# Kernel tuning notes

Measured on AMD Instinct MI355X. Metric: run time of the kernel, lower is better.

Reference implementation:

```python
import jax, jax.numpy as jnp
import numpy as np

N = 20000; E = 160000; C = 64; SH = 9; NB = 8
S_DIM = 16; MS_HID = 64; FC_HID = 64
RATE = 0.1; LAMBDA = 0.5; R_MAX = 5.0; EV_PER = 16
K = int(RATE * N)          # static master-node count (top-k selection)
E_V = EV_PER * K           # static virtual-edge budget


def _safe_len(vec):
    # smooth norm, safe under autodiff at zero-length edges (self loops)
    return jnp.sqrt(jnp.sum(vec * vec, axis=-1, keepdims=True) + 1e-12)


def _sh(vec):
    # real spherical harmonics lmax=2, 'component' normalization, on unit vectors
    n = vec / _safe_len(vec)
    x, y, z = n[:, 0], n[:, 1], n[:, 2]
    s3 = jnp.sqrt(3.0); s15 = jnp.sqrt(15.0); s5 = jnp.sqrt(5.0)
    return jnp.stack([
        jnp.ones_like(x),
        s3 * x, s3 * y, s3 * z,
        s15 * x * y, s15 * y * z, 0.5 * s5 * (3 * z * z - 1.0),
        s15 * x * z, 0.5 * s15 * (x * x - y * y),
    ], axis=-1)  # [E, 9]


def _bessel(r):
    # Bessel radial basis with p=6 polynomial cutoff envelope; r: [E,1]
    n = jnp.arange(1, NB + 1, dtype=r.dtype)
    b = jnp.sqrt(2.0 / R_MAX) * jnp.sin(n * jnp.pi * r / R_MAX) / jnp.clip(r, 1e-9)
    u = jnp.clip(r / R_MAX, 0.0, 1.0); p = 6.0
    env = 1.0 - (p + 1) * (p + 2) / 2 * u ** p + p * (p + 2) * u ** (p + 1) - p * (p + 1) / 2 * u ** (p + 2)
    return b * env  # [E, NB]


def _conv(h, src, dst, sh, ef, emask, n_nodes, fc_w1, fc_b1, fc_w2, fc_b2, lin_w):
    # TFN-style tensor-product conv: per-edge weights from radial MLP,
    # message = flatten(h[dst] outer sh) * w -> linear -> scatter-mean to src
    w = jax.nn.relu(ef @ fc_w1 + fc_b1) @ fc_w2 + fc_b2            # [E, C*SH]
    tp = (h[dst][:, :, None] * sh[:, None, :]).reshape(sh.shape[0], -1) * w
    msg = (tp @ lin_w) * emask[:, None]                            # [E, C]
    agg = jax.ops.segment_sum(msg, src, num_segments=n_nodes)
    deg = jax.ops.segment_sum(emask, src, num_segments=n_nodes)
    return agg / jnp.clip(deg, 1.0)[:, None]


def setup_inputs() -> dict:
    key = jax.random.key(0)
    ks = jax.random.split(key, 12)
    def lin(k, i, o):
        return (jax.random.normal(k, (i, o), jnp.float32) / np.sqrt(i)).astype(jnp.float32)
    return {
        "h": jax.random.normal(ks[0], (N, C), jnp.float32),
        "pos": jax.random.uniform(ks[1], (N, 3), jnp.float32) * 10.0,
        "edge_index": jax.random.randint(ks[2], (2, E), 0, N, dtype=jnp.int32),
        "fc_w1": lin(ks[3], NB, FC_HID), "fc_b1": jnp.zeros((FC_HID,), jnp.float32),
        "fc_w2": lin(ks[4], FC_HID, C * SH), "fc_b2": jnp.zeros((C * SH,), jnp.float32),
        "lin_w": lin(ks[5], C * SH, C),
        "ms_w1": lin(ks[6], S_DIM, MS_HID), "ms_b1": jnp.zeros((MS_HID,), jnp.float32),
        "ms_w2": lin(ks[7], MS_HID, 1), "ms_b2": jnp.zeros((1,), jnp.float32),
        "vg_wq": lin(ks[8], S_DIM, S_DIM), "vg_wk": lin(ks[9], S_DIM, S_DIM),
    }


def reference(h, pos, fc_w1, fc_b1, fc_w2, fc_b2, lin_w,
              ms_w1, ms_b1, ms_w2, ms_b2, vg_wq, vg_wk, edge_index):
    src, dst = edge_index[0], edge_index[1]
    vec = pos[src] - pos[dst]
    sh = _sh(vec)
    ef = _bessel(_safe_len(vec))
    ones_e = jnp.ones((E,), h.dtype)
    h_update = _conv(h, src, dst, sh, ef, ones_e, N, fc_w1, fc_b1, fc_w2, fc_b2, lin_w)
    h_local = h_update + h  # in_dim == out_dim -> pad is a no-op

    # --- master selection (top-k by learned score; static K) ---
    h_sc = h_local[:, :S_DIM]
    score = jax.nn.sigmoid(
        (jax.nn.relu(h_sc @ ms_w1 + ms_b1) @ ms_w2 + ms_b2).squeeze(-1))  # [N]
    _, top_idx = jax.lax.top_k(score, K)
    node_mask = jnp.zeros((N,), h.dtype).at[top_idx].set(1.0)
    m = score * node_mask
    master_idx = jnp.sort(top_idx)

    # relabel full-graph ids -> master-subgraph ids (masked subgraph extraction)
    node2m = jnp.full((N,), -1, jnp.int32).at[master_idx].set(jnp.arange(K, dtype=jnp.int32))
    src_m, dst_m = node2m[src], node2m[dst]
    e_mask = ((src_m >= 0) & (dst_m >= 0)).astype(h.dtype)
    src_mc = jnp.where(src_m >= 0, src_m, 0)
    dst_mc = jnp.where(dst_m >= 0, dst_m, 0)
    adj = jnp.zeros((K, K), h.dtype).at[src_mc, dst_mc].add(e_mask)

    h_master = h_local[master_idx]
    pos_master = pos[master_idx]
    h_ms = h_master[:, :S_DIM]

    # --- virtual edge generation (attention, thresholded by lambda) ---
    q = h_ms @ vg_wq; kk = h_ms @ vg_wk
    attn = jax.nn.sigmoid(q @ kk.T / np.sqrt(S_DIM))  # [K, K]
    exist = (adj > 0) | jnp.eye(K, dtype=bool)
    A_virtual = jnp.where((~exist) & (attn > LAMBDA), 1.0, 0.0).astype(h.dtype)
    vvals, vidx = jax.lax.top_k((attn * A_virtual).reshape(-1), E_V)
    v_src = (vidx // K).astype(jnp.int32); v_dst = (vidx % K).astype(jnp.int32)
    v_mask = (vvals > 0).astype(h.dtype)

    src_all = jnp.concatenate([src_mc, v_src])
    dst_all = jnp.concatenate([dst_mc, v_dst])
    mask_all = jnp.concatenate([e_mask, v_mask])
    vec_m = pos_master[src_all] - pos_master[dst_all]
    sh_m = _sh(vec_m)
    ef_m = _bessel(_safe_len(vec_m))
    h_m_update = _conv(h_master, src_all, dst_all, sh_m, ef_m, mask_all, K,
                       fc_w1, fc_b1, fc_w2, fc_b2, lin_w)
    h_hier = h_m_update + h_master

    h_hier_exp = jnp.zeros_like(h_local).at[master_idx].set(h_hier)
    m_e = m[:, None]
    h_final = (1.0 - m_e) * h_local + m_e * h_hier_exp
    return (h_final, pos, A_virtual, m)
```

## Files before the change

### kernel.cpp

```cpp
#include <hip/hip_runtime.h>
#include <stdint.h>

constexpr int N_   = 20000;
constexpr int E_   = 160000;
constexpr int C_   = 64;
constexpr int K_   = 2000;
constexpr int EV_  = 32000;
constexpr int EALL_ = E_ + EV_;
constexpr int CSH_ = 576;
constexpr int TB_  = 48;

constexpr size_t OFF_AGG    = 0;
constexpr size_t OFF_DEG    = 5120000;
constexpr size_t OFF_AGGM   = 5200000;
constexpr size_t OFF_DEGM   = 5712000;
constexpr size_t OFF_RANK   = 5720000;
constexpr size_t OFF_MASKA  = 5800000;
constexpr size_t OFF_EXIST  = 6568000;
constexpr size_t OFF_HIST   = 10568000;
constexpr size_t OFF_STATE  = 10572096;
constexpr size_t ZERO_BYTES = 10572352;
constexpr size_t OFF_HLOCAL = 10572352;
constexpr size_t OFF_KEY    = 15692352;
constexpr size_t OFF_SCORE  = 15852352;
constexpr size_t OFF_N2M    = 15932352;
constexpr size_t OFF_MIDX   = 16012352;
constexpr size_t OFF_HM     = 16020352;
constexpr size_t OFF_POSM   = 16532352;
constexpr size_t OFF_Q      = 16556352;
constexpr size_t OFF_KBUF   = 16684352;
constexpr size_t OFF_SRCA   = 16812352;
constexpr size_t OFF_DSTA   = 17580352;
constexpr size_t OFF_TMAX   = 18348352;
constexpr size_t OFF_CAND   = 18410880;

struct RState {
    unsigned long long prefix;
    int R;
    unsigned int cand_count;
    unsigned int sel_count;
    int bin_thresh;
    unsigned int total;
    unsigned int pad;
};

__global__ void k_w0(const float* __restrict__ fc_b1, const float* __restrict__ fc_w2,
                     const float* __restrict__ fc_b2, int* __restrict__ w0nz)
{
    __shared__ float hid0[64];
    __shared__ int nz;
    int tid = threadIdx.x;
    if (tid == 0) nz = 0;
    if (tid < 64) hid0[tid] = fmaxf(fc_b1[tid], 0.0f);
    __syncthreads();
    if (tid < CSH_) {
        float acc = fc_b2[tid];
        for (int k = 0; k < 64; k++) acc += hid0[k] * fc_w2[k * CSH_ + tid];
        if (acc != 0.0f) atomicOr(&nz, 1);
    }
    __syncthreads();
    if (tid == 0) *w0nz = nz;
}

__global__ __launch_bounds__(256) void k_prep(
    int n_edges, const int* __restrict__ src, const int* __restrict__ dst,
    const float* __restrict__ mask, const float* __restrict__ posn,
    const int* __restrict__ w0nz, float* __restrict__ deg,
    float* __restrict__ edata, unsigned int* __restrict__ cnt)
{
    int e = blockIdx.x * 256 + threadIdx.x;
    bool valid = e < n_edges;
    int s_i = 0, d_i = 0; float msk = 0.0f;
    if (valid) {
        msk = mask ? mask[e] : 1.0f;
        if (msk != 0.0f) { s_i = src[e]; d_i = dst[e]; }
    }
    bool active = valid && (msk != 0.0f);

    float vx = 0.f, vy = 0.f, vz = 0.f;
    if (active) {
        vx = posn[s_i*3+0] - posn[d_i*3+0];
        vy = posn[s_i*3+1] - posn[d_i*3+1];
        vz = posn[s_i*3+2] - posn[d_i*3+2];
    }
    float r = sqrtf(vx*vx + vy*vy + vz*vz + 1e-12f);
    float invr = 1.0f / r;
    float x = vx*invr, y = vy*invr, z = vz*invr;
    const float s3 = 1.7320508075688772f, s15 = 3.872983346207417f, s5 = 2.23606797749979f;
    float sh[9];
    sh[0] = 1.0f; sh[1] = s3*x; sh[2] = s3*y; sh[3] = s3*z;
    sh[4] = s15*x*y; sh[5] = s15*y*z; sh[6] = 0.5f*s5*(3.0f*z*z - 1.0f);
    sh[7] = s15*x*z; sh[8] = 0.5f*s15*(x*x - y*y);

    float u = r * 0.2f; u = u > 1.0f ? 1.0f : u;
    float u2 = u*u, u6 = u2*u2*u2, u7 = u6*u, u8 = u7*u;
    float env = 1.0f - 28.0f*u6 + 48.0f*u7 - 21.0f*u8;
    float rc = r > 1e-9f ? r : 1e-9f;
    const float bpref = 0.6324555320336759f;
    const float PIov5 = 0.6283185307179586f;
    float ef[8];
    #pragma unroll
    for (int n = 0; n < 8; n++)
        ef[n] = bpref * sinf(PIov5 * r * (float)(n + 1)) / rc * env;

    if (active) atomicAdd(&deg[s_i], msk);

    bool contrib = active && !((env == 0.0f) && (*w0nz == 0));
    int lane = threadIdx.x & 63;
    unsigned long long b = __ballot(contrib);
    int wc = __popcll(b);
    int base = 0;
    if (lane == 0 && wc) base = (int)atomicAdd(cnt, (unsigned)wc);
    base = __shfl(base, 0);
    if (contrib) {
        int slot = base + __popcll(b & ((1ull << lane) - 1ull));
        float* p = edata + (size_t)slot * 20;
        #pragma unroll
        for (int n = 0; n < 8; n++) p[n] = ef[n];
        #pragma unroll
        for (int t = 0; t < 9; t++) p[8+t] = sh[t];
        p[17] = __int_as_float(s_i);
        p[18] = __int_as_float(d_i);
        p[19] = msk;
    }
}

__global__ __launch_bounds__(256, 3) void k_convg(
    const unsigned int* __restrict__ cnt, const float* __restrict__ edata,
    const float* __restrict__ hn,
    const float* __restrict__ fc_w1, const float* __restrict__ fc_b1,
    const float* __restrict__ fc_w2, const float* __restrict__ fc_b2,
    const float* __restrict__ lin_w, float* __restrict__ agg)
{
    __shared__ float s_misc[TB_ * 12];
    __shared__ float s_hid[TB_ * 68];
    __shared__ float s_tp[TB_ * 68];
    __shared__ __align__(16) float s_w[4096];

    const int tid = threadIdx.x;
    const int oq = (tid & 15) * 4;
    const int eg = tid >> 4;

    const int nheavy = (int)*cnt;
    const int nblk = (nheavy + TB_ - 1) / TB_;

    for (int blk = blockIdx.x; blk < nblk; blk += gridDim.x) {
        const int ebase = blk * TB_;
        int nE = nheavy - ebase; if (nE > TB_) nE = TB_;

        __syncthreads();
        for (int idx = tid; idx < TB_ * 12; idx += 256) {
            int e = idx / 12, f = idx - 12 * e;
            float v = 0.0f;
            if (e < nE) {
                const float* p = edata + (size_t)(ebase + e) * 20;
                v = (f < 9) ? p[8 + f] : (f == 9) ? p[17] : (f == 10) ? p[19] : p[18];
            }
            s_misc[idx] = v;
        }
        for (int idx = tid; idx < TB_ * 64; idx += 256) {
            int e = idx >> 6, k = idx & 63;
            float hv = 0.0f;
            if (e < nE) {
                const float* p = edata + (size_t)(ebase + e) * 20;
                float acc = fc_b1[k];
                #pragma unroll
                for (int n = 0; n < 8; n++) acc += p[n] * fc_w1[n * 64 + k];
                hv = fmaxf(acc, 0.0f);
            }
            s_hid[e * 68 + k] = hv;
        }
        float acc0[4] = {0,0,0,0}, acc1[4] = {0,0,0,0}, acc2[4] = {0,0,0,0};
        __syncthreads();

        const int d0 = __float_as_int(s_misc[eg * 12 + 11]);
        const int d1 = __float_as_int(s_misc[(eg + 16) * 12 + 11]);
        const int d2 = __float_as_int(s_misc[(eg + 32) * 12 + 11]);

        for (int cj = 0; cj < 9; cj++) {
            const int j0 = cj * 64;
            if (cj) __syncthreads();
            for (int i4 = tid; i4 < 1024; i4 += 256) {
                int k = i4 >> 4, q4 = (i4 & 15) * 4;
                *reinterpret_cast<float4*>(&s_w[k * 64 + q4]) =
                    *reinterpret_cast<const float4*>(&fc_w2[k * CSH_ + j0 + q4]);
            }
            __syncthreads();

            const int jb = j0 + oq;
            const int c0 = jb / 9, c1 = (jb + 3) / 9;
            float hA0 = hn[d0 * 64 + c0], hB0 = hn[d0 * 64 + c1];
            float hA1 = hn[d1 * 64 + c0], hB1 = hn[d1 * 64 + c1];
            float hA2 = hn[d2 * 64 + c0], hB2 = hn[d2 * 64 + c1];

            float a0[4], a1[4], a2[4];
            #pragma unroll
            for (int q = 0; q < 4; q++) { float b = fc_b2[jb + q]; a0[q]=b; a1[q]=b; a2[q]=b; }
            #pragma unroll 4
            for (int k = 0; k < 64; k++) {
                float4 w4 = *reinterpret_cast<const float4*>(&s_w[k * 64 + oq]);
                float h0 = s_hid[eg * 68 + k];
                float h1 = s_hid[(eg + 16) * 68 + k];
                float h2 = s_hid[(eg + 32) * 68 + k];
                a0[0]+=h0*w4.x; a0[1]+=h0*w4.y; a0[2]+=h0*w4.z; a0[3]+=h0*w4.w;
                a1[0]+=h1*w4.x; a1[1]+=h1*w4.y; a1[2]+=h1*w4.z; a1[3]+=h1*w4.w;
                a2[0]+=h2*w4.x; a2[1]+=h2*w4.y; a2[2]+=h2*w4.z; a2[3]+=h2*w4.w;
            }
            #pragma unroll
            for (int q = 0; q < 4; q++) {
                int j = jb + q; int cc = j / 9; int si = j - 9 * cc;
                s_tp[eg * 68 + oq + q]        = (cc == c0 ? hA0 : hB0) * s_misc[eg * 12 + si]        * a0[q];
                s_tp[(eg + 16) * 68 + oq + q] = (cc == c0 ? hA1 : hB1) * s_misc[(eg + 16) * 12 + si] * a1[q];
                s_tp[(eg + 32) * 68 + oq + q] = (cc == c0 ? hA2 : hB2) * s_misc[(eg + 32) * 12 + si] * a2[q];
            }
            __syncthreads();

            for (int i4 = tid; i4 < 1024; i4 += 256) {
                *reinterpret_cast<float4*>(&s_w[i4 * 4]) =
                    *reinterpret_cast<const float4*>(&lin_w[j0 * 64 + i4 * 4]);
            }
            __syncthreads();

            #pragma unroll 4
            for (int jj = 0; jj < 64; jj++) {
                float4 l4 = *reinterpret_cast<const float4*>(&s_w[jj * 64 + oq]);
                float t0 = s_tp[eg * 68 + jj];
                float t1 = s_tp[(eg + 16) * 68 + jj];
                float t2 = s_tp[(eg + 32) * 68 + jj];
                acc0[0]+=t0*l4.x; acc0[1]+=t0*l4.y; acc0[2]+=t0*l4.z; acc0[3]+=t0*l4.w;
                acc1[0]+=t1*l4.x; acc1[1]+=t1*l4.y; acc1[2]+=t1*l4.z; acc1[3]+=t1*l4.w;
                acc2[0]+=t2*l4.x; acc2[1]+=t2*l4.y; acc2[2]+=t2*l4.z; acc2[3]+=t2*l4.w;
            }
        }

        {
            float mk = s_misc[eg * 12 + 10];
            if (mk != 0.0f) {
                int s = __float_as_int(s_misc[eg * 12 + 9]);
                #pragma unroll
                for (int q = 0; q < 4; q++) atomicAdd(&agg[s * 64 + oq + q], acc0[q] * mk);
            }
            mk = s_misc[(eg + 16) * 12 + 10];
            if (mk != 0.0f) {
                int s = __float_as_int(s_misc[(eg + 16) * 12 + 9]);
                #pragma unroll
                for (int q = 0; q < 4; q++) atomicAdd(&agg[s * 64 + oq + q], acc1[q] * mk);
            }
            mk = s_misc[(eg + 32) * 12 + 10];
            if (mk != 0.0f) {
                int s = __float_as_int(s_misc[(eg + 32) * 12 + 9]);
                #pragma unroll
                for (int q = 0; q < 4; q++) atomicAdd(&agg[s * 64 + oq + q], acc2[q] * mk);
            }
        }
    }
}

__global__ __launch_bounds__(256) void k_hlscore(const float* __restrict__ h,
    const float* __restrict__ agg, const float* __restrict__ deg,
    const float* __restrict__ ms_w1, const float* __restrict__ ms_b1,
    const float* __restrict__ ms_w2, const float* __restrict__ ms_b2,
    float* __restrict__ h_local, float* __restrict__ score, unsigned long long* __restrict__ key)
{
    int wid = threadIdx.x >> 6, lane = threadIdx.x & 63;
    int n = blockIdx.x * 4 + wid;
    if (n >= N_) return;
    float d = fmaxf(deg[n], 1.0f);
    float hl = h[n*64 + lane] + agg[n*64 + lane] / d;
    h_local[n*64 + lane] = hl;
    float acc = ms_b1[lane];
    #pragma unroll
    for (int i = 0; i < 16; i++) acc += __shfl(hl, i) * ms_w1[i*64 + lane];
    acc = fmaxf(acc, 0.0f);
    float part = acc * ms_w2[lane];
    #pragma unroll
    for (int off = 32; off > 0; off >>= 1) part += __shfl_xor(part, off);
    if (lane == 0) {
        float s = part + ms_b2[0];
        float sc = 1.0f / (1.0f + expf(-s));
        score[n] = sc;
        key[n] = ((unsigned long long)__float_as_uint(sc) << 32)
               | (unsigned long long)(0xFFFFFFFFu - (unsigned)n);
    }
}

__global__ __launch_bounds__(256) void k_rank(const unsigned long long* __restrict__ key,
                                              int* __restrict__ rankcnt)
{
    int i = blockIdx.x * 256 + threadIdx.x;
    int seg = blockIdx.y;
    int lo = seg * 1250, hi = lo + 1250;
    unsigned long long my = (i < N_) ? key[i] : ~0ull;
    int cnt = 0;
    #pragma unroll 8
    for (int j = lo; j < hi; j++) cnt += (key[j] > my) ? 1 : 0;
    if (i < N_ && cnt) atomicAdd(&rankcnt[i], cnt);
}

__global__ __launch_bounds__(1024) void k_scanfin(const int* __restrict__ rankcnt,
    const float* __restrict__ score, int* __restrict__ node2m, int* __restrict__ midx,
    float* __restrict__ m_out)
{
    __shared__ int wsum[16];
    __shared__ int wbase[16];
    __shared__ int s_base;
    int tid = threadIdx.x, lane = tid & 63, wv = tid >> 6;
    if (tid == 0) s_base = 0;
    __syncthreads();
    for (int c = 0; c < 20; c++) {
        int idx = c * 1024 + tid;
        int sel = 0;
        if (idx < N_) {
            sel = (rankcnt[idx] < K_) ? 1 : 0;
            m_out[idx] = sel ? score[idx] : 0.0f;
        }
        int v = sel;
        #pragma unroll
        for (int off = 1; off < 64; off <<= 1) {
            int u = __shfl_up(v, off);
            if (lane >= off) v += u;
        }
        if (lane == 63) wsum[wv] = v;
        __syncthreads();
        if (tid == 0) {
            int runb = s_base;
            for (int w = 0; w < 16; w++) { wbase[w] = runb; runb += wsum[w]; }
            s_base = runb;
        }
        __syncthreads();
        if (idx < N_) {
            if (sel) { int rk = wbase[wv] + v - 1; node2m[idx] = rk; midx[rk] = idx; }
            else node2m[idx] = -1;
        }
    }
}

__global__ __launch_bounds__(256) void k_mastex(const int* __restrict__ midx,
    const float* __restrict__ h_local, const float* __restrict__ pos,
    const float* __restrict__ vg_wq, const float* __restrict__ vg_wk,
    const int* __restrict__ src, const int* __restrict__ dst, const int* __restrict__ node2m,
    float* __restrict__ h_m, float* __restrict__ pos_m,
    float* __restrict__ qbuf, float* __restrict__ kbuf,
    int* __restrict__ src_all, int* __restrict__ dst_all,
    float* __restrict__ mask_all, unsigned char* __restrict__ exist)
{
    int b = blockIdx.x;
    if (b < 500) {
        int mi = b * 4 + (threadIdx.x >> 6);
        int lane = threadIdx.x & 63;
        int node = midx[mi];
        h_m[mi*64 + lane] = h_local[node*64 + lane];
        if (lane < 3) pos_m[mi*3 + lane] = pos[node*3 + lane];
        if (lane < 32) {
            int j = lane & 15;
            const float* wm = (lane < 16) ? vg_wq : vg_wk;
            float acc = 0.0f;
            #pragma unroll
            for (int i = 0; i < 16; i++) acc += h_local[node*64 + i] * wm[i*16 + j];
            if (lane < 16) qbuf[mi*16 + j] = acc; else kbuf[mi*16 + j] = acc;
        }
    } else {
        int e = (b - 500) * 256 + threadIdx.x;
        int sm = node2m[src[e]], dm = node2m[dst[e]];
        bool em = (sm >= 0) && (dm >= 0);
        int smc = sm >= 0 ? sm : 0;
        int dmc = dm >= 0 ? dm : 0;
        src_all[e] = smc; dst_all[e] = dmc; mask_all[e] = em ? 1.0f : 0.0f;
        if (em) exist[smc * K_ + dmc] = 1;
    }
}

constexpr int NTILE_ = (K_ / 16) * (K_ / 16);
__global__ __launch_bounds__(256) void k_attn1(const float* __restrict__ qbuf,
    const float* __restrict__ kbuf, const unsigned char* __restrict__ exist,
    float* __restrict__ Av, float* __restrict__ tmax, unsigned int* __restrict__ hist,
    RState* st, unsigned int* __restrict__ done_ctr)
{
    constexpr int TBK = K_ / 16;
    __shared__ float sq[16][17], sk[16][17];
    __shared__ unsigned int lh[1024];
    __shared__ float wmax[4];
    __shared__ unsigned int ha[1024], hb[1024];
    __shared__ unsigned int s_last;
    int tid = threadIdx.x;
    for (int b = tid; b < 1024; b += 256) lh[b] = 0;

    for (int t = blockIdx.x; t < NTILE_; t += gridDim.x) {
        int bi = t / TBK, bj = t % TBK;
        int i0 = bi * 16, j0 = bj * 16;
        int r = tid >> 4, c = tid & 15;
        __syncthreads();
        sq[r][c] = qbuf[(i0 + r) * 16 + c];
        sk[r][c] = kbuf[(j0 + r) * 16 + c];
        __syncthreads();
        int ti = tid >> 4, tj = tid & 15;
        float dot = 0.0f;
        #pragma unroll
        for (int cc = 0; cc < 16; cc++) dot += sq[ti][cc] * sk[tj][cc];
        float attn = 1.0f / (1.0f + expf(-dot * 0.25f));
        int gi = i0 + ti, gj = j0 + tj;
        int flat = gi * K_ + gj;
        bool ex = (exist[flat] != 0) || (gi == gj);
        bool av = (!ex) && (attn > 0.5f);
        Av[flat] = av ? 1.0f : 0.0f;
        float cv = av ? attn : 0.0f;
        if (av) {
            unsigned bin = (__float_as_uint(attn) - 0x3F000000u) >> 13;
            if (bin > 1023u) bin = 1023u;
            atomicAdd(&lh[bin], 1u);
        }
        float wm = cv;
        #pragma unroll
        for (int off = 32; off > 0; off >>= 1) wm = fmaxf(wm, __shfl_xor(wm, off));
        int wid = tid >> 6, lane = tid & 63;
        if (lane == 0) wmax[wid] = wm;
        __syncthreads();
        if (tid == 0) tmax[t] = fmaxf(fmaxf(wmax[0], wmax[1]), fmaxf(wmax[2], wmax[3]));
    }
    __syncthreads();
    for (int b = tid; b < 1024; b += 256) {
        unsigned v = lh[b];
        if (v) atomicAdd(&hist[b], v);
    }
    __syncthreads();
    __threadfence();
    if (tid == 0) s_last = (atomicAdd(done_ctr, 1u) == (unsigned)gridDim.x - 1u) ? 1u : 0u;
    __syncthreads();
    if (!s_last) return;
    __threadfence();
    for (int b = tid; b < 1024; b += 256) ha[b] = hist[b];
    __syncthreads();
    unsigned* srcp = ha; unsigned* dstp = hb;
    for (int off = 1; off < 1024; off <<= 1) {
        for (int b = tid; b < 1024; b += 256)
            dstp[b] = srcp[b] + ((b + off < 1024) ? srcp[b + off] : 0u);
        __syncthreads();
        unsigned* tmp = srcp; srcp = dstp; dstp = tmp;
    }
    unsigned total = srcp[0];
    int R = (total < (unsigned)EV_) ? (int)total : EV_;
    if (tid == 0) {
        st->R = R; st->total = total; st->cand_count = 0; st->sel_count = 0;
        if (R == 0) st->bin_thresh = 1024;
    }
    __syncthreads();
    if (R > 0) {
        for (int b = tid; b < 1024; b += 256) {
            unsigned hi2 = (b == 1023) ? 0u : srcp[b + 1];
            if ((int)srcp[b] >= R && (int)hi2 < R) st->bin_thresh = b;
        }
    }
}

__global__ __launch_bounds__(256) void k_attn2(const float* __restrict__ qbuf,
    const float* __restrict__ kbuf, const unsigned char* __restrict__ exist,
    const float* __restrict__ tmax, RState* st, unsigned long long* __restrict__ cand)
{
    constexpr int TBK = K_ / 16;
    __shared__ float sq[16][17], sk[16][17];
    __shared__ int wb[4];
    __shared__ int bb;
    int tid = threadIdx.x;
    unsigned tbits = 0x3F000000u + ((unsigned)st->bin_thresh << 13);

    for (int t = blockIdx.x; t < NTILE_; t += gridDim.x) {
        if (__float_as_uint(tmax[t]) < tbits) continue;
        int bi = t / TBK, bj = t % TBK;
        int i0 = bi * 16, j0 = bj * 16;
        int r = tid >> 4, c = tid & 15;
        __syncthreads();
        sq[r][c] = qbuf[(i0 + r) * 16 + c];
        sk[r][c] = kbuf[(j0 + r) * 16 + c];
        __syncthreads();
        int ti = tid >> 4, tj = tid & 15;
        float dot = 0.0f;
        #pragma unroll
        for (int cc = 0; cc < 16; cc++) dot += sq[ti][cc] * sk[tj][cc];
        float attn = 1.0f / (1.0f + expf(-dot * 0.25f));
        int gi = i0 + ti, gj = j0 + tj;
        int flat = gi * K_ + gj;
        bool ex = (exist[flat] != 0) || (gi == gj);
        bool store = (!ex) && (attn > 0.5f) && (__float_as_uint(attn) >= tbits);

        unsigned long long keyv = ((unsigned long long)__float_as_uint(attn) << 32)
                                | (unsigned long long)(0xFFFFFFFFu - (unsigned)flat);
        int wid = tid >> 6, lane = tid & 63;
        unsigned long long b = __ballot(store);
        int wc = __popcll(b);
        if (lane == 0) wb[wid] = wc;
        __syncthreads();
        if (tid == 0) {
            int s = 0;
            for (int w = 0; w < 4; w++) { int cc2 = wb[w]; wb[w] = s; s += cc2; }
            bb = s ? (int)atomicAdd(&st->cand_count, (unsigned)s) : 0;
        }
        __syncthreads();
        if (store) {
            int slot = bb + wb[wid] + __popcll(b & ((1ull << lane) - 1ull));
            cand[slot] = keyv;
        }
    }
}

__global__ __launch_bounds__(1024) void k_radixsel(RState* st,
    const unsigned long long* __restrict__ cand,
    int* __restrict__ src_all, int* __restrict__ dst_all, float* __restrict__ mask_all)
{
    __shared__ unsigned int lh[256];
    __shared__ unsigned int suf[256];
    __shared__ unsigned int s_tie[8192];
    __shared__ unsigned int s_pref, s_R, s_tiecnt, s_cfth;
    int tid = threadIdx.x;
    int n = (int)st->cand_count;
    int R = st->R;
    if (tid == 0) { s_pref = 0x3F000000u; s_R = (unsigned)R; s_tiecnt = 0; s_cfth = 0; }
    __syncthreads();

    unsigned long long T;
    if (R > 0) {
        for (int p = 0; p < 3; p++) {
            if (tid < 256) lh[tid] = 0;
            __syncthreads();
            unsigned pref = s_pref;
            int sh_d = 16 - 8 * p;
            unsigned pm = 0xFFFFFFFFu << (sh_d + 8);
            for (int i = tid; i < n; i += 1024) {
                unsigned a = (unsigned)(cand[i] >> 32);
                if ((a & pm) == (pref & pm))
                    atomicAdd(&lh[(a >> sh_d) & 255u], 1u);
            }
            __syncthreads();
            if (tid < 256) suf[tid] = lh[tid];
            __syncthreads();
            for (int off = 1; off < 256; off <<= 1) {
                unsigned v = 0;
                if (tid < 256 && tid + off < 256) v = suf[tid + off];
                __syncthreads();
                if (tid < 256) suf[tid] += v;
                __syncthreads();
            }
            if (tid < 256) {
                unsigned Rc = s_R;
                unsigned hi2 = (tid == 255) ? 0u : suf[tid + 1];
                if (suf[tid] >= Rc && hi2 < Rc) {
                    s_pref = pref | ((unsigned)tid << sh_d);
                    s_R = Rc - hi2;
                }
            }
            __syncthreads();
        }
        unsigned Ta = s_pref;
        unsigned Rrem = s_R;
        for (int i = tid; i < n; i += 1024) {
            unsigned long long kv = cand[i];
            if ((unsigned)(kv >> 32) == Ta) {
                unsigned pos = atomicAdd(&s_tiecnt, 1u);
                if (pos < 8192u) s_tie[pos] = (unsigned)(kv & 0xFFFFFFFFull);
            }
        }
        __syncthreads();
        unsigned Cq = s_tiecnt; if (Cq > 8192u) Cq = 8192u;
        if (Rrem >= 1u && Rrem < Cq) {
            for (int i = tid; i < (int)Cq; i += 1024) {
                unsigned me = s_tie[i];
                unsigned r = 0;
                for (int j = 0; j < (int)Cq; j++) r += (s_tie[j] > me) ? 1u : 0u;
                if (r == Rrem - 1u) s_cfth = me;
            }
        }
        __syncthreads();
        T = ((unsigned long long)Ta << 32) | (unsigned long long)s_cfth;
    } else {
        T = ~0ull;
    }

    int lane = tid & 63;
    for (int i0 = 0; i0 < n; i0 += 1024) {
        int i = i0 + tid;
        bool sel = (i < n) && (cand[i] >= T);
        unsigned long long b = __ballot(sel);
        int wc = __popcll(b);
        int basep = 0;
        if (lane == 0 && wc) basep = (int)atomicAdd(&st->sel_count, (unsigned)wc);
        basep = __shfl(basep, 0);
        if (sel) {
            int slot = basep + __popcll(b & ((1ull << lane) - 1ull));
            if (slot < EV_) {
                unsigned flat = 0xFFFFFFFFu - (unsigned)(cand[i] & 0xFFFFFFFFull);
                src_all[E_ + slot] = (int)(flat / (unsigned)K_);
                dst_all[E_ + slot] = (int)(flat % (unsigned)K_);
                mask_all[E_ + slot] = 1.0f;
            }
        }
    }
}

__global__ void k_finalpos(const float* __restrict__ h_local, const int* __restrict__ node2m,
    const float* __restrict__ aggm, const float* __restrict__ degm, const float* __restrict__ h_m,
    const float* __restrict__ m_out, const float* __restrict__ pos,
    float* __restrict__ out_h, float* __restrict__ out_pos)
{
    int idx = blockIdx.x * 256 + threadIdx.x;
    if (idx < N_ * 3) out_pos[idx] = pos[idx];
    if (idx >= N_ * C_) return;
    int i = idx >> 6, c = idx & 63;
    float mval = m_out[i];
    int mi = node2m[i];
    float hh = 0.0f;
    if (mi >= 0) hh = aggm[mi*64 + c] / fmaxf(degm[mi], 1.0f) + h_m[mi*64 + c];
    out_h[idx] = (1.0f - mval) * h_local[idx] + mval * hh;
}

extern "C" void kernel_launch(void* const* d_in, const int* in_sizes, int n_in,
                              void* d_out, int out_size, void* d_ws, size_t ws_size,
                              hipStream_t stream)
{
    (void)in_sizes; (void)n_in; (void)out_size; (void)ws_size;
    const float* h     = (const float*)d_in[0];
    const float* pos   = (const float*)d_in[1];
    const int*   eidx  = (const int*)d_in[2];
    const float* fc_w1 = (const float*)d_in[3];
    const float* fc_b1 = (const float*)d_in[4];
    const float* fc_w2 = (const float*)d_in[5];
    const float* fc_b2 = (const float*)d_in[6];
    const float* lin_w = (const float*)d_in[7];
    const float* ms_w1 = (const float*)d_in[8];
    const float* ms_b1 = (const float*)d_in[9];
    const float* ms_w2 = (const float*)d_in[10];
    const float* ms_b2 = (const float*)d_in[11];
    const float* vg_wq = (const float*)d_in[12];
    const float* vg_wk = (const float*)d_in[13];

    char* ws = (char*)d_ws;
    float* agg     = (float*)(ws + OFF_AGG);
    float* deg     = (float*)(ws + OFF_DEG);
    float* aggm    = (float*)(ws + OFF_AGGM);
    float* degm    = (float*)(ws + OFF_DEGM);
    int*   rankcnt = (int*)(ws + OFF_RANK);
    float* mask_all = (float*)(ws + OFF_MASKA);
    unsigned char* exist = (unsigned char*)(ws + OFF_EXIST);
    unsigned int* hist = (unsigned int*)(ws + OFF_HIST);
    RState* st     = (RState*)(ws + OFF_STATE);
    unsigned int* cnt0 = (unsigned int*)(ws + OFF_STATE + 64);
    unsigned int* cnt1 = (unsigned int*)(ws + OFF_STATE + 68);
    int*   w0nz    = (int*)(ws + OFF_STATE + 72);
    unsigned int* done_ctr = (unsigned int*)(ws + OFF_STATE + 76);
    float* h_local = (float*)(ws + OFF_HLOCAL);
    unsigned long long* key = (unsigned long long*)(ws + OFF_KEY);
    float* score   = (float*)(ws + OFF_SCORE);
    int*   node2m  = (int*)(ws + OFF_N2M);
    int*   midx    = (int*)(ws + OFF_MIDX);
    float* h_m     = (float*)(ws + OFF_HM);
    float* pos_m   = (float*)(ws + OFF_POSM);
    float* qbuf    = (float*)(ws + OFF_Q);
    float* kbuf    = (float*)(ws + OFF_KBUF);
    int*   src_all = (int*)(ws + OFF_SRCA);
    int*   dst_all = (int*)(ws + OFF_DSTA);
    float* tmax    = (float*)(ws + OFF_TMAX);
    unsigned long long* cand = (unsigned long long*)(ws + OFF_CAND);
    float* edata   = (float*)(ws + OFF_CAND);

    float* out_h   = (float*)d_out;
    float* out_pos = out_h + (size_t)N_ * C_;
    float* out_av  = out_pos + (size_t)N_ * 3;
    float* out_m   = out_av + (size_t)K_ * K_;

    hipMemsetAsync(ws, 0, ZERO_BYTES, stream);

    k_w0<<<1, 576, 0, stream>>>(fc_b1, fc_w2, fc_b2, w0nz);

    k_prep<<<E_ / 256, 256, 0, stream>>>(E_, eidx, eidx + E_, nullptr, pos, w0nz, deg, edata, cnt0);
    k_convg<<<768, 256, 0, stream>>>(cnt0, edata, h, fc_w1, fc_b1, fc_w2, fc_b2, lin_w, agg);

    k_hlscore<<<(N_ + 3) / 4, 256, 0, stream>>>(h, agg, deg, ms_w1, ms_b1, ms_w2, ms_b2,
                                                h_local, score, key);

    k_rank<<<dim3((N_ + 255) / 256, 16), 256, 0, stream>>>(key, rankcnt);
    k_scanfin<<<1, 1024, 0, stream>>>(rankcnt, score, node2m, midx, out_m);

    k_mastex<<<500 + E_ / 256, 256, 0, stream>>>(midx, h_local, pos, vg_wq, vg_wk,
        eidx, eidx + E_, node2m, h_m, pos_m, qbuf, kbuf, src_all, dst_all, mask_all, exist);

    k_attn1<<<1024, 256, 0, stream>>>(qbuf, kbuf, exist, out_av, tmax, hist, st, done_ctr);
    k_attn2<<<1024, 256, 0, stream>>>(qbuf, kbuf, exist, tmax, st, cand);
    k_radixsel<<<1, 1024, 0, stream>>>(st, cand, src_all, dst_all, mask_all);

    k_prep<<<EALL_ / 256, 256, 0, stream>>>(EALL_, src_all, dst_all, mask_all, pos_m, w0nz,
                                            degm, edata, cnt1);
    k_convg<<<768, 256, 0, stream>>>(cnt1, edata, h_m, fc_w1, fc_b1, fc_w2, fc_b2, lin_w, aggm);

    k_finalpos<<<(N_ * C_ + 255) / 256, 256, 0, stream>>>(h_local, node2m, aggm, degm, h_m,
                                                          out_m, pos, out_h, out_pos);
}
```

Before: 744.2 us.

## Fuse all pipeline stages into one cooperative megakernel with grid syncs

Merges the memset, weight-check, edge-prep, conv, scoring, ranking, selection, attention and final stages into one cooperatively launched kernel of 768 blocks, separated by grid-wide barriers. The single-block serial scan for master selection is replaced by a three-phase parallel count, block-base scan and emit. The goal is to remove per-launch overhead and idle gaps between many small kernels. The cost is a grid sync at each stage boundary, one shared-memory and register budget that fits every stage, and a fallback to separate per-stage launches if the cooperative launch fails.

```diff
diff --git a/kernel.cpp b/kernel.cpp
--- a/kernel.cpp
+++ b/kernel.cpp
@@ -1,5 +1,7 @@
 #include <hip/hip_runtime.h>
+#include <hip/hip_cooperative_groups.h>
 #include <stdint.h>
+namespace cg = cooperative_groups;
 
 constexpr int N_   = 20000;
 constexpr int E_   = 160000;
@@ -9,6 +11,9 @@
 constexpr int EALL_ = E_ + EV_;
 constexpr int CSH_ = 576;
 constexpr int TB_  = 48;
+constexpr int GRID_ = 768;
+constexpr int NTILE_ = (K_ / 16) * (K_ / 16);
+constexpr int SPAN_ = 27;
 
 constexpr size_t OFF_AGG    = 0;
 constexpr size_t OFF_DEG    = 5120000;
@@ -18,21 +23,23 @@
 constexpr size_t OFF_MASKA  = 5800000;
 constexpr size_t OFF_EXIST  = 6568000;
 constexpr size_t OFF_HIST   = 10568000;
-constexpr size_t OFF_STATE  = 10572096;
-constexpr size_t ZERO_BYTES = 10572352;
-constexpr size_t OFF_HLOCAL = 10572352;
-constexpr size_t OFF_KEY    = 15692352;
-constexpr size_t OFF_SCORE  = 15852352;
-constexpr size_t OFF_N2M    = 15932352;
-constexpr size_t OFF_MIDX   = 16012352;
-constexpr size_t OFF_HM     = 16020352;
-constexpr size_t OFF_POSM   = 16532352;
-constexpr size_t OFF_Q      = 16556352;
-constexpr size_t OFF_KBUF   = 16684352;
-constexpr size_t OFF_SRCA   = 16812352;
-constexpr size_t OFF_DSTA   = 17580352;
-constexpr size_t OFF_TMAX   = 18348352;
-constexpr size_t OFF_CAND   = 18410880;
+constexpr size_t OFF_BSUM   = 10572096;
+constexpr size_t OFF_BBASE  = 10575168;
+constexpr size_t OFF_STATE  = 10578240;
+constexpr size_t ZERO_MAIN  = OFF_STATE;
+constexpr size_t OFF_HLOCAL = 10578496;
+constexpr size_t OFF_KEY    = 15698496;
+constexpr size_t OFF_SCORE  = 15858496;
+constexpr size_t OFF_N2M    = 15938496;
+constexpr size_t OFF_MIDX   = 16018496;
+constexpr size_t OFF_HM     = 16026496;
+constexpr size_t OFF_POSM   = 16538496;
+constexpr size_t OFF_Q      = 16562496;
+constexpr size_t OFF_KBUF   = 16690496;
+constexpr size_t OFF_SRCA   = 16818496;
+constexpr size_t OFF_DSTA   = 17586496;
+constexpr size_t OFF_TMAX   = 18354496;
+constexpr size_t OFF_CAND   = 18417024;
 
 struct RState {
     unsigned long long prefix;
@@ -44,30 +51,49 @@
     unsigned int pad;
 };
 
-__global__ void k_w0(const float* __restrict__ fc_b1, const float* __restrict__ fc_w2,
-                     const float* __restrict__ fc_b2, int* __restrict__ w0nz)
-{
-    __shared__ float hid0[64];
-    __shared__ int nz;
-    int tid = threadIdx.x;
-    if (tid == 0) nz = 0;
-    if (tid < 64) hid0[tid] = fmaxf(fc_b1[tid], 0.0f);
-    __syncthreads();
-    if (tid < CSH_) {
-        float acc = fc_b2[tid];
-        for (int k = 0; k < 64; k++) acc += hid0[k] * fc_w2[k * CSH_ + tid];
-        if (acc != 0.0f) atomicOr(&nz, 1);
-    }
-    __syncthreads();
-    if (tid == 0) *w0nz = nz;
-}
-
-__global__ __launch_bounds__(256) void k_prep(
-    int n_edges, const int* __restrict__ src, const int* __restrict__ dst,
-    const float* __restrict__ mask, const float* __restrict__ posn,
-    const int* __restrict__ w0nz, float* __restrict__ deg,
+struct P {
+    const float* h; const float* pos; const int* eidx;
+    const float* fc_w1; const float* fc_b1; const float* fc_w2; const float* fc_b2;
+    const float* lin_w; const float* ms_w1; const float* ms_b1; const float* ms_w2;
+    const float* ms_b2; const float* vg_wq; const float* vg_wk;
+    char* ws;
+    float* out_h; float* out_pos; float* out_av; float* out_m;
+};
+
+constexpr int SMEM_BYTES = 44800;
+
+
+__device__ void st0_init(const P& p, char* smem)
+{
+    float4 zero4 = make_float4(0.f, 0.f, 0.f, 0.f);
+    float4* z = (float4*)p.ws;
+    int nz4 = (int)(ZERO_MAIN / 16);
+    for (int i = blockIdx.x * 256 + threadIdx.x; i < nz4; i += GRID_ * 256) z[i] = zero4;
+    if (blockIdx.x == GRID_ - 1) {
+        int t = threadIdx.x;
+        float4* zs = (float4*)(p.ws + OFF_STATE);
+        if (t < 16) zs[t] = zero4;
+        float* hid0 = (float*)smem;
+        int* nz = (int*)(smem + 256);
+        if (t == 0) *nz = 0;
+        if (t < 64) hid0[t] = fmaxf(p.fc_b1[t], 0.0f);
+        __syncthreads();
+        for (int j = t; j < CSH_; j += 256) {
+            float acc = p.fc_b2[j];
+            for (int k = 0; k < 64; k++) acc += hid0[k] * p.fc_w2[k * CSH_ + j];
+            if (acc != 0.0f) atomicOr(nz, 1);
+        }
+        __syncthreads();
+        if (t == 0) *(int*)(p.ws + OFF_STATE + 72) = *nz;
+    }
+}
+
+__device__ void prep_stage(const P& p, int n_edges, const int* __restrict__ src,
+    const int* __restrict__ dst, const float* __restrict__ mask,
+    const float* __restrict__ posn, float* __restrict__ deg,
     float* __restrict__ edata, unsigned int* __restrict__ cnt)
 {
+    int w0flag = *(const int*)(p.ws + OFF_STATE + 72);
     int e = blockIdx.x * 256 + threadIdx.x;
     bool valid = e < n_edges;
     int s_i = 0, d_i = 0; float msk = 0.0f;
@@ -105,7 +131,7 @@
 
     if (active) atomicAdd(&deg[s_i], msk);
 
-    bool contrib = active && !((env == 0.0f) && (*w0nz == 0));
+    bool contrib = active && !((env == 0.0f) && (w0flag == 0));
     int lane = threadIdx.x & 63;
     unsigned long long b = __ballot(contrib);
     int wc = __popcll(b);
@@ -114,28 +140,24 @@
     base = __shfl(base, 0);
     if (contrib) {
         int slot = base + __popcll(b & ((1ull << lane) - 1ull));
-        float* p = edata + (size_t)slot * 20;
+        float* pp = edata + (size_t)slot * 20;
         #pragma unroll
-        for (int n = 0; n < 8; n++) p[n] = ef[n];
+        for (int n = 0; n < 8; n++) pp[n] = ef[n];
         #pragma unroll
-        for (int t = 0; t < 9; t++) p[8+t] = sh[t];
-        p[17] = __int_as_float(s_i);
-        p[18] = __int_as_float(d_i);
-        p[19] = msk;
-    }
-}
-
-__global__ __launch_bounds__(256, 3) void k_convg(
-    const unsigned int* __restrict__ cnt, const float* __restrict__ edata,
-    const float* __restrict__ hn,
-    const float* __restrict__ fc_w1, const float* __restrict__ fc_b1,
-    const float* __restrict__ fc_w2, const float* __restrict__ fc_b2,
-    const float* __restrict__ lin_w, float* __restrict__ agg)
-{
-    __shared__ float s_misc[TB_ * 12];
-    __shared__ float s_hid[TB_ * 68];
-    __shared__ float s_tp[TB_ * 68];
-    __shared__ __align__(16) float s_w[4096];
+        for (int t = 0; t < 9; t++) pp[8+t] = sh[t];
+        pp[17] = __int_as_float(s_i);
+        pp[18] = __int_as_float(d_i);
+        pp[19] = msk;
+    }
+}
+
+__device__ void st_conv(const P& p, char* smem, const unsigned int* __restrict__ cnt,
+    const float* __restrict__ edata, const float* __restrict__ hn, float* __restrict__ agg)
+{
+    float* s_misc = (float*)smem;
+    float* s_hid  = (float*)(smem + 2304);
+    float* s_tp   = (float*)(smem + 15360);
+    float* s_w    = (float*)(smem + 28416);
 
     const int tid = threadIdx.x;
     const int oq = (tid & 15) * 4;
@@ -144,7 +166,7 @@
     const int nheavy = (int)*cnt;
     const int nblk = (nheavy + TB_ - 1) / TB_;
 
-    for (int blk = blockIdx.x; blk < nblk; blk += gridDim.x) {
+    for (int blk = blockIdx.x; blk < nblk; blk += GRID_) {
         const int ebase = blk * TB_;
         int nE = nheavy - ebase; if (nE > TB_) nE = TB_;
 
@@ -153,8 +175,8 @@
             int e = idx / 12, f = idx - 12 * e;
             float v = 0.0f;
             if (e < nE) {
-                const float* p = edata + (size_t)(ebase + e) * 20;
-                v = (f < 9) ? p[8 + f] : (f == 9) ? p[17] : (f == 10) ? p[19] : p[18];
+                const float* pp = edata + (size_t)(ebase + e) * 20;
+                v = (f < 9) ? pp[8 + f] : (f == 9) ? pp[17] : (f == 10) ? pp[19] : pp[18];
             }
             s_misc[idx] = v;
         }
@@ -162,10 +184,10 @@
             int e = idx >> 6, k = idx & 63;
             float hv = 0.0f;
             if (e < nE) {
-                const float* p = edata + (size_t)(ebase + e) * 20;
-                float acc = fc_b1[k];
+                const float* pp = edata + (size_t)(ebase + e) * 20;
+                float acc = p.fc_b1[k];
                 #pragma unroll
-                for (int n = 0; n < 8; n++) acc += p[n] * fc_w1[n * 64 + k];
+                for (int n = 0; n < 8; n++) acc += pp[n] * p.fc_w1[n * 64 + k];
                 hv = fmaxf(acc, 0.0f);
             }
             s_hid[e * 68 + k] = hv;
@@ -183,7 +205,7 @@
             for (int i4 = tid; i4 < 1024; i4 += 256) {
                 int k = i4 >> 4, q4 = (i4 & 15) * 4;
                 *reinterpret_cast<float4*>(&s_w[k * 64 + q4]) =
-                    *reinterpret_cast<const float4*>(&fc_w2[k * CSH_ + j0 + q4]);
+                    *reinterpret_cast<const float4*>(&p.fc_w2[k * CSH_ + j0 + q4]);
             }
             __syncthreads();
 
@@ -195,7 +217,7 @@
 
             float a0[4], a1[4], a2[4];
             #pragma unroll
-            for (int q = 0; q < 4; q++) { float b = fc_b2[jb + q]; a0[q]=b; a1[q]=b; a2[q]=b; }
+            for (int q = 0; q < 4; q++) { float b = p.fc_b2[jb + q]; a0[q]=b; a1[q]=b; a2[q]=b; }
             #pragma unroll 4
             for (int k = 0; k < 64; k++) {
                 float4 w4 = *reinterpret_cast<const float4*>(&s_w[k * 64 + oq]);
@@ -217,7 +239,7 @@
 
             for (int i4 = tid; i4 < 1024; i4 += 256) {
                 *reinterpret_cast<float4*>(&s_w[i4 * 4]) =
-                    *reinterpret_cast<const float4*>(&lin_w[j0 * 64 + i4 * 4]);
+                    *reinterpret_cast<const float4*>(&p.lin_w[j0 * 64 + i4 * 4]);
             }
             __syncthreads();
 
@@ -256,111 +278,145 @@
     }
 }
 
-__global__ __launch_bounds__(256) void k_hlscore(const float* __restrict__ h,
-    const float* __restrict__ agg, const float* __restrict__ deg,
-    const float* __restrict__ ms_w1, const float* __restrict__ ms_b1,
-    const float* __restrict__ ms_w2, const float* __restrict__ ms_b2,
-    float* __restrict__ h_local, float* __restrict__ score, unsigned long long* __restrict__ key)
-{
-    int wid = threadIdx.x >> 6, lane = threadIdx.x & 63;
-    int n = blockIdx.x * 4 + wid;
-    if (n >= N_) return;
-    float d = fmaxf(deg[n], 1.0f);
-    float hl = h[n*64 + lane] + agg[n*64 + lane] / d;
-    h_local[n*64 + lane] = hl;
-    float acc = ms_b1[lane];
+__device__ void st3_hlscore(const P& p)
+{
+    const float* agg = (const float*)(p.ws + OFF_AGG);
+    const float* deg = (const float*)(p.ws + OFF_DEG);
+    float* h_local = (float*)(p.ws + OFF_HLOCAL);
+    float* score = (float*)(p.ws + OFF_SCORE);
+    unsigned long long* key = (unsigned long long*)(p.ws + OFF_KEY);
+    int lane = threadIdx.x & 63;
+    int gw = (blockIdx.x * 256 + threadIdx.x) >> 6;
+    for (int n = gw; n < N_; n += GRID_ * 4) {
+        float d = fmaxf(deg[n], 1.0f);
+        float hl = p.h[n*64 + lane] + agg[n*64 + lane] / d;
+        h_local[n*64 + lane] = hl;
+        float acc = p.ms_b1[lane];
+        #pragma unroll
+        for (int i = 0; i < 16; i++) acc += __shfl(hl, i) * p.ms_w1[i*64 + lane];
+        acc = fmaxf(acc, 0.0f);
+        float part = acc * p.ms_w2[lane];
+        #pragma unroll
+        for (int off = 32; off > 0; off >>= 1) part += __shfl_xor(part, off);
+        if (lane == 0) {
+            float s = part + p.ms_b2[0];
+            float sc = 1.0f / (1.0f + expf(-s));
+            score[n] = sc;
+            key[n] = ((unsigned long long)__float_as_uint(sc) << 32)
+                   | (unsigned long long)(0xFFFFFFFFu - (unsigned)n);
+        }
+    }
+}
+
+__device__ void st4_rank(const P& p)
+{
+    const unsigned long long* key = (const unsigned long long*)(p.ws + OFF_KEY);
+    int* rankcnt = (int*)(p.ws + OFF_RANK);
+    int tid = threadIdx.x;
+    for (int unit = blockIdx.x; unit < 79 * 16; unit += GRID_) {
+        int i = (unit % 79) * 256 + tid;
+        int seg = unit / 79;
+        int lo = seg * 1250, hi = lo + 1250;
+        unsigned long long my = (i < N_) ? key[i] : ~0ull;
+        int cnt = 0;
+        #pragma unroll 8
+        for (int j = lo; j < hi; j++) cnt += (key[j] > my) ? 1 : 0;
+        if (i < N_ && cnt) atomicAdd(&rankcnt[i], cnt);
+    }
+}
+
+__device__ void st5a_count(const P& p)
+{
+    const int* rankcnt = (const int*)(p.ws + OFF_RANK);
+    const float* score = (const float*)(p.ws + OFF_SCORE);
+    int* bsum = (int*)(p.ws + OFF_BSUM);
+    if (threadIdx.x < 64) {
+        int lane = threadIdx.x;
+        int idx = blockIdx.x * SPAN_ + lane;
+        bool in = (lane < SPAN_) && (idx < N_);
+        int sel = 0;
+        if (in) {
+            sel = (rankcnt[idx] < K_) ? 1 : 0;
+            p.out_m[idx] = sel ? score[idx] : 0.0f;
+        }
+        unsigned long long bal = __ballot(sel);
+        if (lane == 0) bsum[blockIdx.x] = __popcll(bal);
+    }
+}
+
+__device__ void st5b_base(const P& p, char* smem)
+{
+    int* bsum = (int*)(p.ws + OFF_BSUM);
+    int* bbase = (int*)(p.ws + OFF_BBASE);
+    int t = threadIdx.x, lane = t & 63, wv = t >> 6;
+    int a0 = bsum[3*t], a1 = bsum[3*t+1], a2 = bsum[3*t+2];
+    int local = a0 + a1 + a2;
+    int v = local;
     #pragma unroll
-    for (int i = 0; i < 16; i++) acc += __shfl(hl, i) * ms_w1[i*64 + lane];
-    acc = fmaxf(acc, 0.0f);
-    float part = acc * ms_w2[lane];
-    #pragma unroll
-    for (int off = 32; off > 0; off >>= 1) part += __shfl_xor(part, off);
-    if (lane == 0) {
-        float s = part + ms_b2[0];
-        float sc = 1.0f / (1.0f + expf(-s));
-        score[n] = sc;
-        key[n] = ((unsigned long long)__float_as_uint(sc) << 32)
-               | (unsigned long long)(0xFFFFFFFFu - (unsigned)n);
-    }
-}
-
-__global__ __launch_bounds__(256) void k_rank(const unsigned long long* __restrict__ key,
-                                              int* __restrict__ rankcnt)
-{
-    int i = blockIdx.x * 256 + threadIdx.x;
-    int seg = blockIdx.y;
-    int lo = seg * 1250, hi = lo + 1250;
-    unsigned long long my = (i < N_) ? key[i] : ~0ull;
-    int cnt = 0;
-    #pragma unroll 8
-    for (int j = lo; j < hi; j++) cnt += (key[j] > my) ? 1 : 0;
-    if (i < N_ && cnt) atomicAdd(&rankcnt[i], cnt);
-}
-
-__global__ __launch_bounds__(1024) void k_scanfin(const int* __restrict__ rankcnt,
-    const float* __restrict__ score, int* __restrict__ node2m, int* __restrict__ midx,
-    float* __restrict__ m_out)
-{
-    __shared__ int wsum[16];
-    __shared__ int wbase[16];
-    __shared__ int s_base;
-    int tid = threadIdx.x, lane = tid & 63, wv = tid >> 6;
-    if (tid == 0) s_base = 0;
+    for (int off = 1; off < 64; off <<= 1) {
+        int u = __shfl_up(v, off);
+        if (lane >= off) v += u;
+    }
+    int* wsums = (int*)smem;
+    if (lane == 63) wsums[wv] = v;
     __syncthreads();
-    for (int c = 0; c < 20; c++) {
-        int idx = c * 1024 + tid;
-        int sel = 0;
-        if (idx < N_) {
-            sel = (rankcnt[idx] < K_) ? 1 : 0;
-            m_out[idx] = sel ? score[idx] : 0.0f;
-        }
-        int v = sel;
-        #pragma unroll
-        for (int off = 1; off < 64; off <<= 1) {
-            int u = __shfl_up(v, off);
-            if (lane >= off) v += u;
-        }
-        if (lane == 63) wsum[wv] = v;
-        __syncthreads();
-        if (tid == 0) {
-            int runb = s_base;
-            for (int w = 0; w < 16; w++) { wbase[w] = runb; runb += wsum[w]; }
-            s_base = runb;
-        }
-        __syncthreads();
-        if (idx < N_) {
-            if (sel) { int rk = wbase[wv] + v - 1; node2m[idx] = rk; midx[rk] = idx; }
+    if (t == 0) { int run = 0; for (int w = 0; w < 4; w++) { int c = wsums[w]; wsums[w] = run; run += c; } }
+    __syncthreads();
+    int excl = wsums[wv] + v - local;
+    bbase[3*t] = excl; bbase[3*t+1] = excl + a0; bbase[3*t+2] = excl + a0 + a1;
+}
+
+__device__ void st5c_emitmap(const P& p)
+{
+    const int* rankcnt = (const int*)(p.ws + OFF_RANK);
+    const int* bbase = (const int*)(p.ws + OFF_BBASE);
+    int* node2m = (int*)(p.ws + OFF_N2M);
+    int* midx = (int*)(p.ws + OFF_MIDX);
+    if (threadIdx.x < 64) {
+        int lane = threadIdx.x;
+        int idx = blockIdx.x * SPAN_ + lane;
+        bool in = (lane < SPAN_) && (idx < N_);
+        int sel = in ? ((rankcnt[idx] < K_) ? 1 : 0) : 0;
+        unsigned long long bal = __ballot(sel);
+        int pre = __popcll(bal & ((1ull << lane) - 1ull));
+        if (in) {
+            if (sel) { int rk = bbase[blockIdx.x] + pre; node2m[idx] = rk; midx[rk] = idx; }
             else node2m[idx] = -1;
         }
     }
 }
 
-__global__ __launch_bounds__(256) void k_mastex(const int* __restrict__ midx,
-    const float* __restrict__ h_local, const float* __restrict__ pos,
-    const float* __restrict__ vg_wq, const float* __restrict__ vg_wk,
-    const int* __restrict__ src, const int* __restrict__ dst, const int* __restrict__ node2m,
-    float* __restrict__ h_m, float* __restrict__ pos_m,
-    float* __restrict__ qbuf, float* __restrict__ kbuf,
-    int* __restrict__ src_all, int* __restrict__ dst_all,
-    float* __restrict__ mask_all, unsigned char* __restrict__ exist)
-{
-    int b = blockIdx.x;
-    if (b < 500) {
-        int mi = b * 4 + (threadIdx.x >> 6);
-        int lane = threadIdx.x & 63;
+__device__ void st6_mastex(const P& p)
+{
+    const int* midx = (const int*)(p.ws + OFF_MIDX);
+    const float* h_local = (const float*)(p.ws + OFF_HLOCAL);
+    const int* node2m = (const int*)(p.ws + OFF_N2M);
+    float* h_m = (float*)(p.ws + OFF_HM);
+    float* pos_m = (float*)(p.ws + OFF_POSM);
+    float* qbuf = (float*)(p.ws + OFF_Q);
+    float* kbuf = (float*)(p.ws + OFF_KBUF);
+    int* src_all = (int*)(p.ws + OFF_SRCA);
+    int* dst_all = (int*)(p.ws + OFF_DSTA);
+    float* mask_all = (float*)(p.ws + OFF_MASKA);
+    unsigned char* exist = (unsigned char*)(p.ws + OFF_EXIST);
+    const int* src = p.eidx; const int* dst = p.eidx + E_;
+
+    int lane = threadIdx.x & 63;
+    int gw = (blockIdx.x * 256 + threadIdx.x) >> 6;
+    for (int mi = gw; mi < K_; mi += GRID_ * 4) {
         int node = midx[mi];
         h_m[mi*64 + lane] = h_local[node*64 + lane];
-        if (lane < 3) pos_m[mi*3 + lane] = pos[node*3 + lane];
+        if (lane < 3) pos_m[mi*3 + lane] = p.pos[node*3 + lane];
         if (lane < 32) {
             int j = lane & 15;
-            const float* wm = (lane < 16) ? vg_wq : vg_wk;
+            const float* wm = (lane < 16) ? p.vg_wq : p.vg_wk;
             float acc = 0.0f;
             #pragma unroll
             for (int i = 0; i < 16; i++) acc += h_local[node*64 + i] * wm[i*16 + j];
             if (lane < 16) qbuf[mi*16 + j] = acc; else kbuf[mi*16 + j] = acc;
         }
-    } else {
-        int e = (b - 500) * 256 + threadIdx.x;
+    }
+    for (int e = blockIdx.x * 256 + threadIdx.x; e < E_; e += GRID_ * 256) {
         int sm = node2m[src[e]], dm = node2m[dst[e]];
         bool em = (sm >= 0) && (dm >= 0);
         int smc = sm >= 0 ? sm : 0;
@@ -370,22 +426,22 @@
     }
 }
 
-constexpr int NTILE_ = (K_ / 16) * (K_ / 16);
-__global__ __launch_bounds__(256) void k_attn1(const float* __restrict__ qbuf,
-    const float* __restrict__ kbuf, const unsigned char* __restrict__ exist,
-    float* __restrict__ Av, float* __restrict__ tmax, unsigned int* __restrict__ hist,
-    RState* st, unsigned int* __restrict__ done_ctr)
-{
+__device__ void st7a_attn1(const P& p, char* smem)
+{
+    const float* qbuf = (const float*)(p.ws + OFF_Q);
+    const float* kbuf = (const float*)(p.ws + OFF_KBUF);
+    const unsigned char* exist = (const unsigned char*)(p.ws + OFF_EXIST);
+    float* tmax = (float*)(p.ws + OFF_TMAX);
+    unsigned int* hist = (unsigned int*)(p.ws + OFF_HIST);
+    float (*sq)[17] = (float(*)[17])smem;
+    float (*sk)[17] = (float(*)[17])(smem + 1088);
+    unsigned int* lh = (unsigned int*)(smem + 2176);
+    float* wmax = (float*)(smem + 6272);
     constexpr int TBK = K_ / 16;
-    __shared__ float sq[16][17], sk[16][17];
-    __shared__ unsigned int lh[1024];
-    __shared__ float wmax[4];
-    __shared__ unsigned int ha[1024], hb[1024];
-    __shared__ unsigned int s_last;
     int tid = threadIdx.x;
     for (int b = tid; b < 1024; b += 256) lh[b] = 0;
 
-    for (int t = blockIdx.x; t < NTILE_; t += gridDim.x) {
+    for (int t = blockIdx.x; t < NTILE_; t += GRID_) {
         int bi = t / TBK, bj = t % TBK;
         int i0 = bi * 16, j0 = bj * 16;
         int r = tid >> 4, c = tid & 15;
@@ -402,7 +458,7 @@
         int flat = gi * K_ + gj;
         bool ex = (exist[flat] != 0) || (gi == gj);
         bool av = (!ex) && (attn > 0.5f);
-        Av[flat] = av ? 1.0f : 0.0f;
+        p.out_av[flat] = av ? 1.0f : 0.0f;
         float cv = av ? attn : 0.0f;
         if (av) {
             unsigned bin = (__float_as_uint(attn) - 0x3F000000u) >> 13;
@@ -422,12 +478,15 @@
         unsigned v = lh[b];
         if (v) atomicAdd(&hist[b], v);
     }
-    __syncthreads();
-    __threadfence();
-    if (tid == 0) s_last = (atomicAdd(done_ctr, 1u) == (unsigned)gridDim.x - 1u) ? 1u : 0u;
-    __syncthreads();
-    if (!s_last) return;
-    __threadfence();
+}
+
+__device__ void st7b_bsel(const P& p, char* smem)
+{
+    const unsigned int* hist = (const unsigned int*)(p.ws + OFF_HIST);
+    RState* st = (RState*)(p.ws + OFF_STATE);
+    unsigned int* ha = (unsigned int*)smem;
+    unsigned int* hb = (unsigned int*)(smem + 4096);
+    int tid = threadIdx.x;
     for (int b = tid; b < 1024; b += 256) ha[b] = hist[b];
     __syncthreads();
     unsigned* srcp = ha; unsigned* dstp = hb;
@@ -452,18 +511,23 @@
     }
 }
 
-__global__ __launch_bounds__(256) void k_attn2(const float* __restrict__ qbuf,
-    const float* __restrict__ kbuf, const unsigned char* __restrict__ exist,
-    const float* __restrict__ tmax, RState* st, unsigned long long* __restrict__ cand)
-{
+__device__ void st8_attn2(const P& p, char* smem)
+{
+    const float* qbuf = (const float*)(p.ws + OFF_Q);
+    const float* kbuf = (const float*)(p.ws + OFF_KBUF);
+    const unsigned char* exist = (const unsigned char*)(p.ws + OFF_EXIST);
+    const float* tmax = (const float*)(p.ws + OFF_TMAX);
+    RState* st = (RState*)(p.ws + OFF_STATE);
+    unsigned long long* cand = (unsigned long long*)(p.ws + OFF_CAND);
+    float (*sq)[17] = (float(*)[17])smem;
+    float (*sk)[17] = (float(*)[17])(smem + 1088);
+    int* wb = (int*)(smem + 2176);
+    int* bbp = (int*)(smem + 2192);
     constexpr int TBK = K_ / 16;
-    __shared__ float sq[16][17], sk[16][17];
-    __shared__ int wb[4];
-    __shared__ int bb;
     int tid = threadIdx.x;
     unsigned tbits = 0x3F000000u + ((unsigned)st->bin_thresh << 13);
 
-    for (int t = blockIdx.x; t < NTILE_; t += gridDim.x) {
+    for (int t = blockIdx.x; t < NTILE_; t += GRID_) {
         if (__float_as_uint(tmax[t]) < tbits) continue;
         int bi = t / TBK, bj = t % TBK;
         int i0 = bi * 16, j0 = bj * 16;
@@ -492,91 +556,101 @@
         if (tid == 0) {
             int s = 0;
             for (int w = 0; w < 4; w++) { int cc2 = wb[w]; wb[w] = s; s += cc2; }
-            bb = s ? (int)atomicAdd(&st->cand_count, (unsigned)s) : 0;
+            *bbp = s ? (int)atomicAdd(&st->cand_count, (unsigned)s) : 0;
         }
         __syncthreads();
         if (store) {
-            int slot = bb + wb[wid] + __popcll(b & ((1ull << lane) - 1ull));
+            int slot = *bbp + wb[wid] + __popcll(b & ((1ull << lane) - 1ull));
             cand[slot] = keyv;
         }
     }
 }
 
-__global__ __launch_bounds__(1024) void k_radixsel(RState* st,
-    const unsigned long long* __restrict__ cand,
-    int* __restrict__ src_all, int* __restrict__ dst_all, float* __restrict__ mask_all)
-{
-    __shared__ unsigned int lh[256];
-    __shared__ unsigned int suf[256];
-    __shared__ unsigned int s_tie[8192];
-    __shared__ unsigned int s_pref, s_R, s_tiecnt, s_cfth;
+__device__ void st9a_radix(const P& p, char* smem)
+{
+    RState* st = (RState*)(p.ws + OFF_STATE);
+    const unsigned long long* cand = (const unsigned long long*)(p.ws + OFF_CAND);
+    unsigned int* s_tie = (unsigned int*)smem;
+    unsigned int* lh = (unsigned int*)(smem + 32768);
+    unsigned int* suf = (unsigned int*)(smem + 33792);
+    unsigned int* scal = (unsigned int*)(smem + 34816);
     int tid = threadIdx.x;
     int n = (int)st->cand_count;
     int R = st->R;
-    if (tid == 0) { s_pref = 0x3F000000u; s_R = (unsigned)R; s_tiecnt = 0; s_cfth = 0; }
+    if (tid == 0) { scal[0] = 0x3F000000u; scal[1] = (unsigned)R; scal[2] = 0; scal[3] = 0; }
     __syncthreads();
 
     unsigned long long T;
     if (R > 0) {
-        for (int p = 0; p < 3; p++) {
-            if (tid < 256) lh[tid] = 0;
+        for (int pss = 0; pss < 3; pss++) {
+            lh[tid] = 0;
             __syncthreads();
-            unsigned pref = s_pref;
-            int sh_d = 16 - 8 * p;
+            unsigned pref = scal[0];
+            int sh_d = 16 - 8 * pss;
             unsigned pm = 0xFFFFFFFFu << (sh_d + 8);
-            for (int i = tid; i < n; i += 1024) {
+            for (int i = tid; i < n; i += 256) {
                 unsigned a = (unsigned)(cand[i] >> 32);
                 if ((a & pm) == (pref & pm))
                     atomicAdd(&lh[(a >> sh_d) & 255u], 1u);
             }
             __syncthreads();
-            if (tid < 256) suf[tid] = lh[tid];
+            suf[tid] = lh[tid];
             __syncthreads();
             for (int off = 1; off < 256; off <<= 1) {
-                unsigned v = 0;
-                if (tid < 256 && tid + off < 256) v = suf[tid + off];
+                unsigned v = (tid + off < 256) ? suf[tid + off] : 0u;
                 __syncthreads();
-                if (tid < 256) suf[tid] += v;
+                suf[tid] += v;
                 __syncthreads();
             }
-            if (tid < 256) {
-                unsigned Rc = s_R;
+            {
+                unsigned Rc = scal[1];
                 unsigned hi2 = (tid == 255) ? 0u : suf[tid + 1];
                 if (suf[tid] >= Rc && hi2 < Rc) {
-                    s_pref = pref | ((unsigned)tid << sh_d);
-                    s_R = Rc - hi2;
+                    scal[0] = pref | ((unsigned)tid << sh_d);
+                    scal[1] = Rc - hi2;
                 }
             }
             __syncthreads();
         }
-        unsigned Ta = s_pref;
-        unsigned Rrem = s_R;
-        for (int i = tid; i < n; i += 1024) {
+        unsigned Ta = scal[0];
+        unsigned Rrem = scal[1];
+        for (int i = tid; i < n; i += 256) {
             unsigned long long kv = cand[i];
             if ((unsigned)(kv >> 32) == Ta) {
-                unsigned pos = atomicAdd(&s_tiecnt, 1u);
+                unsigned pos = atomicAdd(&scal[2], 1u);
                 if (pos < 8192u) s_tie[pos] = (unsigned)(kv & 0xFFFFFFFFull);
             }
         }
         __syncthreads();
-        unsigned Cq = s_tiecnt; if (Cq > 8192u) Cq = 8192u;
+        unsigned Cq = scal[2]; if (Cq > 8192u) Cq = 8192u;
         if (Rrem >= 1u && Rrem < Cq) {
-            for (int i = tid; i < (int)Cq; i += 1024) {
+            for (int i = tid; i < (int)Cq; i += 256) {
                 unsigned me = s_tie[i];
                 unsigned r = 0;
                 for (int j = 0; j < (int)Cq; j++) r += (s_tie[j] > me) ? 1u : 0u;
-                if (r == Rrem - 1u) s_cfth = me;
-            }
-        }
-        __syncthreads();
-        T = ((unsigned long long)Ta << 32) | (unsigned long long)s_cfth;
+                if (r == Rrem - 1u) scal[3] = me;
+            }
+        }
+        __syncthreads();
+        T = ((unsigned long long)Ta << 32) | (unsigned long long)scal[3];
     } else {
         T = ~0ull;
     }
-
-    int lane = tid & 63;
-    for (int i0 = 0; i0 < n; i0 += 1024) {
-        int i = i0 + tid;
+    if (tid == 0) st->prefix = T;
+}
+
+__device__ void st9b_emit(const P& p)
+{
+    RState* st = (RState*)(p.ws + OFF_STATE);
+    const unsigned long long* cand = (const unsigned long long*)(p.ws + OFF_CAND);
+    int* src_all = (int*)(p.ws + OFF_SRCA);
+    int* dst_all = (int*)(p.ws + OFF_DSTA);
+    float* mask_all = (float*)(p.ws + OFF_MASKA);
+    int n = (int)st->cand_count;
+    unsigned long long T = st->prefix;
+    int lane = threadIdx.x & 63;
+    for (int i0 = blockIdx.x * 256; i0 < n; i0 += GRID_ * 256) {
+        int i = i0 + threadIdx.x;
         bool sel = (i < n) && (cand[i] >= T);
         unsigned long long b = __ballot(sel);
         int wc = __popcll(b);
@@ -595,100 +669,144 @@
     }
 }
 
-__global__ void k_finalpos(const float* __restrict__ h_local, const int* __restrict__ node2m,
-    const float* __restrict__ aggm, const float* __restrict__ degm, const float* __restrict__ h_m,
-    const float* __restrict__ m_out, const float* __restrict__ pos,
-    float* __restrict__ out_h, float* __restrict__ out_pos)
-{
-    int idx = blockIdx.x * 256 + threadIdx.x;
-    if (idx < N_ * 3) out_pos[idx] = pos[idx];
-    if (idx >= N_ * C_) return;
-    int i = idx >> 6, c = idx & 63;
-    float mval = m_out[i];
-    int mi = node2m[i];
-    float hh = 0.0f;
-    if (mi >= 0) hh = aggm[mi*64 + c] / fmaxf(degm[mi], 1.0f) + h_m[mi*64 + c];
-    out_h[idx] = (1.0f - mval) * h_local[idx] + mval * hh;
-}
+__device__ void st12_final(const P& p)
+{
+    const float* h_local = (const float*)(p.ws + OFF_HLOCAL);
+    const int* node2m = (const int*)(p.ws + OFF_N2M);
+    const float* aggm = (const float*)(p.ws + OFF_AGGM);
+    const float* degm = (const float*)(p.ws + OFF_DEGM);
+    const float* h_m = (const float*)(p.ws + OFF_HM);
+    for (int idx = blockIdx.x * 256 + threadIdx.x; idx < N_ * C_; idx += GRID_ * 256) {
+        if (idx < N_ * 3) p.out_pos[idx] = p.pos[idx];
+        int i = idx >> 6, c = idx & 63;
+        float mval = p.out_m[i];
+        int mi = node2m[i];
+        float hh = 0.0f;
+        if (mi >= 0) hh = aggm[mi*64 + c] / fmaxf(degm[mi], 1.0f) + h_m[mi*64 + c];
+        p.out_h[idx] = (1.0f - mval) * h_local[idx] + mval * hh;
+    }
+}
+
+__global__ __launch_bounds__(256, 3) void k_mega(P p)
+{
+    cg::grid_group grid = cg::this_grid();
+    __shared__ __align__(16) char smem[SMEM_BYTES];
+    unsigned int* cnt0 = (unsigned int*)(p.ws + OFF_STATE + 64);
+    unsigned int* cnt1 = (unsigned int*)(p.ws + OFF_STATE + 68);
+    float* edata = (float*)(p.ws + OFF_CAND);
+    float* agg = (float*)(p.ws + OFF_AGG);
+    float* deg = (float*)(p.ws + OFF_DEG);
+    float* aggm = (float*)(p.ws + OFF_AGGM);
+    float* degm = (float*)(p.ws + OFF_DEGM);
+    float* h_m = (float*)(p.ws + OFF_HM);
+    float* pos_m = (float*)(p.ws + OFF_POSM);
+    int* src_all = (int*)(p.ws + OFF_SRCA);
+    int* dst_all = (int*)(p.ws + OFF_DSTA);
+    float* mask_all = (float*)(p.ws + OFF_MASKA);
+
+    st0_init(p, smem);                                                  grid.sync();
+    prep_stage(p, E_, p.eidx, p.eidx + E_, nullptr, p.pos, deg, edata, cnt0);  grid.sync();
+    st_conv(p, smem, cnt0, edata, p.h, agg);                            grid.sync();
+    st3_hlscore(p);                                                     grid.sync();
+    st4_rank(p);                                                        grid.sync();
+    st5a_count(p);                                                      grid.sync();
+    if (blockIdx.x == 0) st5b_base(p, smem);                            grid.sync();
+    st5c_emitmap(p);                                                    grid.sync();
+    st6_mastex(p);                                                      grid.sync();
+    st7a_attn1(p, smem);                                                grid.sync();
+    if (blockIdx.x == 0) st7b_bsel(p, smem);                            grid.sync();
+    st8_attn2(p, smem);                                                 grid.sync();
+    if (blockIdx.x == 0) st9a_radix(p, smem);                           grid.sync();
+    st9b_emit(p);                                                       grid.sync();
+    prep_stage(p, EALL_, src_all, dst_all, mask_all, pos_m, degm, edata, cnt1); grid.sync();
+    st_conv(p, smem, cnt1, edata, h_m, aggm);                           grid.sync();
+    st12_final(p);
+}
+
+#define SMEMDECL __shared__ __align__(16) char smem[SMEM_BYTES]
+__global__ __launch_bounds__(256, 3) void k_s0(P p) { SMEMDECL; st0_init(p, smem); }
+__global__ __launch_bounds__(256, 3) void k_s1(P p) {
+    prep_stage(p, E_, p.eidx, p.eidx + E_, nullptr, p.pos,
+               (float*)(p.ws + OFF_DEG), (float*)(p.ws + OFF_CAND),
+               (unsigned int*)(p.ws + OFF_STATE + 64));
+}
+__global__ __launch_bounds__(256, 3) void k_s2(P p) {
+    SMEMDECL;
+    st_conv(p, smem, (const unsigned int*)(p.ws + OFF_STATE + 64),
+            (const float*)(p.ws + OFF_CAND), p.h, (float*)(p.ws + OFF_AGG));
+}
+__global__ __launch_bounds__(256, 3) void k_s3(P p) { st3_hlscore(p); }
+__global__ __launch_bounds__(256, 3) void k_s4(P p) { st4_rank(p); }
+__global__ __launch_bounds__(256, 3) void k_s5a(P p) { st5a_count(p); }
+__global__ __launch_bounds__(256, 3) void k_s5b(P p) { SMEMDECL; if (blockIdx.x == 0) st5b_base(p, smem); }
+__global__ __launch_bounds__(256, 3) void k_s5c(P p) { st5c_emitmap(p); }
+__global__ __launch_bounds__(256, 3) void k_s6(P p) { st6_mastex(p); }
+__global__ __launch_bounds__(256, 3) void k_s7a(P p) { SMEMDECL; st7a_attn1(p, smem); }
+__global__ __launch_bounds__(256, 3) void k_s7b(P p) { SMEMDECL; if (blockIdx.x == 0) st7b_bsel(p, smem); }
+__global__ __launch_bounds__(256, 3) void k_s8(P p) { SMEMDECL; st8_attn2(p, smem); }
+__global__ __launch_bounds__(256, 3) void k_s9a(P p) { SMEMDECL; if (blockIdx.x == 0) st9a_radix(p, smem); }
+__global__ __launch_bounds__(256, 3) void k_s9b(P p) { st9b_emit(p); }
+__global__ __launch_bounds__(256, 3) void k_s10(P p) {
+    prep_stage(p, EALL_, (const int*)(p.ws + OFF_SRCA), (const int*)(p.ws + OFF_DSTA),
+               (const float*)(p.ws + OFF_MASKA), (const float*)(p.ws + OFF_POSM),
+               (float*)(p.ws + OFF_DEGM), (float*)(p.ws + OFF_CAND),
+               (unsigned int*)(p.ws + OFF_STATE + 68));
+}
+__global__ __launch_bounds__(256, 3) void k_s11(P p) {
+    SMEMDECL;
+    st_conv(p, smem, (const unsigned int*)(p.ws + OFF_STATE + 68),
+            (const float*)(p.ws + OFF_CAND), (const float*)(p.ws + OFF_HM),
+            (float*)(p.ws + OFF_AGGM));
+}
+__global__ __launch_bounds__(256, 3) void k_s12(P p) { st12_final(p); }
 
 extern "C" void kernel_launch(void* const* d_in, const int* in_sizes, int n_in,
                               void* d_out, int out_size, void* d_ws, size_t ws_size,
                               hipStream_t stream)
 {
     (void)in_sizes; (void)n_in; (void)out_size; (void)ws_size;
-    const float* h     = (const float*)d_in[0];
-    const float* pos   = (const float*)d_in[1];
-    const int*   eidx  = (const int*)d_in[2];
-    const float* fc_w1 = (const float*)d_in[3];
-    const float* fc_b1 = (const float*)d_in[4];
-    const float* fc_w2 = (const float*)d_in[5];
-    const float* fc_b2 = (const float*)d_in[6];
-    const float* lin_w = (const float*)d_in[7];
-    const float* ms_w1 = (const float*)d_in[8];
-    const float* ms_b1 = (const float*)d_in[9];
-    const float* ms_w2 = (const float*)d_in[10];
-    const float* ms_b2 = (const float*)d_in[11];
-    const float* vg_wq = (const float*)d_in[12];
-    const float* vg_wk = (const float*)d_in[13];
-
-    char* ws = (char*)d_ws;
-    float* agg     = (float*)(ws + OFF_AGG);
-    float* deg     = (float*)(ws + OFF_DEG);
-    float* aggm    = (float*)(ws + OFF_AGGM);
-    float* degm    = (float*)(ws + OFF_DEGM);
-    int*   rankcnt = (int*)(ws + OFF_RANK);
-    float* mask_all = (float*)(ws + OFF_MASKA);
-    unsigned char* exist = (unsigned char*)(ws + OFF_EXIST);
-    unsigned int* hist = (unsigned int*)(ws + OFF_HIST);
-    RState* st     = (RState*)(ws + OFF_STATE);
-    unsigned int* cnt0 = (unsigned int*)(ws + OFF_STATE + 64);
-    unsigned int* cnt1 = (unsigned int*)(ws + OFF_STATE + 68);
-    int*   w0nz    = (int*)(ws + OFF_STATE + 72);
-    unsigned int* done_ctr = (unsigned int*)(ws + OFF_STATE + 76);
-    float* h_local = (float*)(ws + OFF_HLOCAL);
-    unsigned long long* key = (unsigned long long*)(ws + OFF_KEY);
-    float* score   = (float*)(ws + OFF_SCORE);
-    int*   node2m  = (int*)(ws + OFF_N2M);
-    int*   midx    = (int*)(ws + OFF_MIDX);
-    float* h_m     = (float*)(ws + OFF_HM);
-    float* pos_m   = (float*)(ws + OFF_POSM);
-    float* qbuf    = (float*)(ws + OFF_Q);
-    float* kbuf    = (float*)(ws + OFF_KBUF);
-    int*   src_all = (int*)(ws + OFF_SRCA);
-    int*   dst_all = (int*)(ws + OFF_DSTA);
-    float* tmax    = (float*)(ws + OFF_TMAX);
-    unsigned long long* cand = (unsigned long long*)(ws + OFF_CAND);
-    float* edata   = (float*)(ws + OFF_CAND);
-
-    float* out_h   = (float*)d_out;
-    float* out_pos = out_h + (size_t)N_ * C_;
-    float* out_av  = out_pos + (size_t)N_ * 3;
-    float* out_m   = out_av + (size_t)K_ * K_;
-
-    hipMemsetAsync(ws, 0, ZERO_BYTES, stream);
-
-    k_w0<<<1, 576, 0, stream>>>(fc_b1, fc_w2, fc_b2, w0nz);
-
-    k_prep<<<E_ / 256, 256, 0, stream>>>(E_, eidx, eidx + E_, nullptr, pos, w0nz, deg, edata, cnt0);
-    k_convg<<<768, 256, 0, stream>>>(cnt0, edata, h, fc_w1, fc_b1, fc_w2, fc_b2, lin_w, agg);
-
-    k_hlscore<<<(N_ + 3) / 4, 256, 0, stream>>>(h, agg, deg, ms_w1, ms_b1, ms_w2, ms_b2,
-                                                h_local, score, key);
-
-    k_rank<<<dim3((N_ + 255) / 256, 16), 256, 0, stream>>>(key, rankcnt);
-    k_scanfin<<<1, 1024, 0, stream>>>(rankcnt, score, node2m, midx, out_m);
-
-    k_mastex<<<500 + E_ / 256, 256, 0, stream>>>(midx, h_local, pos, vg_wq, vg_wk,
-        eidx, eidx + E_, node2m, h_m, pos_m, qbuf, kbuf, src_all, dst_all, mask_all, exist);
-
-    k_attn1<<<1024, 256, 0, stream>>>(qbuf, kbuf, exist, out_av, tmax, hist, st, done_ctr);
-    k_attn2<<<1024, 256, 0, stream>>>(qbuf, kbuf, exist, tmax, st, cand);
-    k_radixsel<<<1, 1024, 0, stream>>>(st, cand, src_all, dst_all, mask_all);
-
-    k_prep<<<EALL_ / 256, 256, 0, stream>>>(EALL_, src_all, dst_all, mask_all, pos_m, w0nz,
-                                            degm, edata, cnt1);
-    k_convg<<<768, 256, 0, stream>>>(cnt1, edata, h_m, fc_w1, fc_b1, fc_w2, fc_b2, lin_w, aggm);
-
-    k_finalpos<<<(N_ * C_ + 255) / 256, 256, 0, stream>>>(h_local, node2m, aggm, degm, h_m,
-                                                          out_m, pos, out_h, out_pos);
-}
+    P p;
+    p.h     = (const float*)d_in[0];
+    p.pos   = (const float*)d_in[1];
+    p.eidx  = (const int*)d_in[2];
+    p.fc_w1 = (const float*)d_in[3];
+    p.fc_b1 = (const float*)d_in[4];
+    p.fc_w2 = (const float*)d_in[5];
+    p.fc_b2 = (const float*)d_in[6];
+    p.lin_w = (const float*)d_in[7];
+    p.ms_w1 = (const float*)d_in[8];
+    p.ms_b1 = (const float*)d_in[9];
+    p.ms_w2 = (const float*)d_in[10];
+    p.ms_b2 = (const float*)d_in[11];
+    p.vg_wq = (const float*)d_in[12];
+    p.vg_wk = (const float*)d_in[13];
+    p.ws    = (char*)d_ws;
+    p.out_h   = (float*)d_out;
+    p.out_pos = p.out_h + (size_t)N_ * C_;
+    p.out_av  = p.out_pos + (size_t)N_ * 3;
+    p.out_m   = p.out_av + (size_t)K_ * K_;
+
+    void* args[] = { &p };
+    hipError_t err = hipLaunchCooperativeKernel((const void*)k_mega, dim3(GRID_), dim3(256),
+                                                args, 0, stream);
+    if (err != hipSuccess) {
+        (void)hipGetLastError();
+        k_s0 <<<GRID_, 256, 0, stream>>>(p);
+        k_s1 <<<GRID_, 256, 0, stream>>>(p);
+        k_s2 <<<GRID_, 256, 0, stream>>>(p);
+        k_s3 <<<GRID_, 256, 0, stream>>>(p);
+        k_s4 <<<GRID_, 256, 0, stream>>>(p);
+        k_s5a<<<GRID_, 256, 0, stream>>>(p);
+        k_s5b<<<GRID_, 256, 0, stream>>>(p);
+        k_s5c<<<GRID_, 256, 0, stream>>>(p);
+        k_s6 <<<GRID_, 256, 0, stream>>>(p);
+        k_s7a<<<GRID_, 256, 0, stream>>>(p);
+        k_s7b<<<GRID_, 256, 0, stream>>>(p);
+        k_s8 <<<GRID_, 256, 0, stream>>>(p);
+        k_s9a<<<GRID_, 256, 0, stream>>>(p);
+        k_s9b<<<GRID_, 256, 0, stream>>>(p);
+        k_s10<<<GRID_, 256, 0, stream>>>(p);
+        k_s11<<<GRID_, 256, 0, stream>>>(p);
+        k_s12<<<GRID_, 256, 0, stream>>>(p);
+    }
+}
```

After: 2.112 ms. +183.8%, slower.
